# Performance work log

Hardware: AMD Instinct MI355X
Metric: run time of the kernel (lower is better)

Reference implementation:

```python
import jax, jax.numpy as jnp
import numpy as np

B, L, H, E = 16, 4096, 8, 64
IN_CH, OUT_CH, MODES = 512, 512, 64


def setup_inputs() -> dict:
    key = jax.random.key(0)
    kq, kk, kv, k1, k2 = jax.random.split(key, 5)
    scale = 1.0 / (IN_CH * OUT_CH)
    q = jax.random.normal(kq, (B, L, H, E), jnp.float32)
    k = jax.random.normal(kk, (B, L, H, E), jnp.float32)
    v = jax.random.normal(kv, (B, L, H, E), jnp.float32)
    mask = jnp.zeros((B, L), jnp.bool_)
    # learned params: (heads=8, in_ch//8, out_ch//8, modes), torch.rand init * scale
    w1 = scale * jax.random.uniform(k1, (8, IN_CH // 8, OUT_CH // 8, MODES), jnp.float32)
    w2 = scale * jax.random.uniform(k2, (8, IN_CH // 8, OUT_CH // 8, MODES), jnp.float32)
    return {"q": q, "k": k, "v": v, "mask": mask, "w1": w1, "w2": w2}


def reference(q, k, v, mask, w1, w2):
    # q: [B, L, H, E]; k, v, mask unused by the original forward.
    Bq, Lq, Hq, Eq = q.shape
    modes = w1.shape[-1]
    x = jnp.transpose(q, (0, 2, 3, 1))          # [B, H, E, L]
    x_ft = jnp.fft.rfft(x, axis=-1)             # [B, H, E, L//2+1] complex64
    # mode_select_method='else' => index = [0..modes-1], wi == i, so the
    # per-mode gather/einsum/scatter loop collapses to a slice + batched einsum.
    sel = x_ft[..., :modes]                     # [B, H, E_in, modes]
    wc = w1 + 1j * w2                           # [H, E_in, E_out, modes] complex
    out_modes = jnp.einsum('bhim,hiom->bhom', sel, wc)  # [B, H, E_out, modes]
    nfreq = Lq // 2 + 1
    out_ft = jnp.zeros((Bq, Hq, w1.shape[2], nfreq), jnp.complex64)
    out_ft = out_ft.at[..., :modes].set(out_modes)
    x_out = jnp.fft.irfft(out_ft, n=Lq, axis=-1)  # [B, H, E_out, L] float32
    return x_out
```

## Files before the change

kernel.cpp:

```cpp
#include <hip/hip_runtime.h>
#include <math.h>

#define NB 16
#define NL 4096
#define NH 8
#define NI 64
#define NO 64
#define NM 64
#define STEP 1.5339807878856412e-3f

using bf16_t = __bf16;
using bf16x8 = __attribute__((ext_vector_type(8))) __bf16;
using f32x16 = __attribute__((ext_vector_type(16))) float;

#define LDW 136
#define TMC 128

__global__ __launch_bounds__(256) void k_tab(bf16_t* __restrict__ Thi,
                                             bf16_t* __restrict__ Tlo,
                                             bf16_t* __restrict__ Tfhi,
                                             bf16_t* __restrict__ Tflo) {
  const int gid = blockIdx.x * 256 + threadIdx.x;
  {
    const int l = gid >> 7, mc = gid & 127, m = mc >> 1;
    const int p = (m * l) & 4095;
    const float c = cosf((float)p * STEP);
    const float s = cosf((float)((p + 3072) & 4095) * STEP);
    const float val = (mc & 1) ? -s : c;
    const bf16_t hi = (bf16_t)val;
    Thi[gid] = hi;
    Tlo[gid] = (bf16_t)(val - (float)hi);
  }
  {
    const int mc = gid >> 12, l = gid & 4095, m = mc >> 1;
    const int p = (m * l) & 4095;
    const float c = cosf((float)p * STEP);
    const float s = cosf((float)((p + 3072) & 4095) * STEP);
    const float val = (mc & 1) ? -s : c;
    const bf16_t hi = (bf16_t)val;
    Tfhi[gid] = hi;
    Tflo[gid] = (bf16_t)(val - (float)hi);
  }
}

__global__ __launch_bounds__(256) void k_fwd(const float* __restrict__ q,
                                             float* __restrict__ partial,
                                             const bf16_t* __restrict__ Tfhi,
                                             const bf16_t* __restrict__ Tflo,
                                             int LCF, int KCH) {
  const int lc = blockIdx.x, h = blockIdx.y, b = blockIdx.z;
  const int t = threadIdx.x;
  __shared__ uint32_t Bh[64][33], Bl[64][33];

  const int w = t >> 6, lane = t & 63;
  const int arow = lane & 31;
  const int kh = (lane >> 5) << 3;
  const int lp = t & 31;
  const int i0 = (t >> 5) << 3;

  f32x16 acc[2] = {};

  const int lbase0 = lc * KCH;
  const bf16_t* Ah = Tfhi + (size_t)(w * 32 + arow) * NL + lbase0 + kh;
  const bf16_t* Al = Tflo + (size_t)(w * 32 + arow) * NL + lbase0 + kh;

  for (int ks = 0; ks < KCH; ks += 64) {
    __syncthreads();
    {
      const int l0 = lbase0 + ks + (lp << 1);
      const float* qp = q + (((size_t)b * NL + l0) * NH + h) * NI + i0;
      const float4 a0 = *(const float4*)qp;
      const float4 a1 = *(const float4*)(qp + 4);
      const float4 b0 = *(const float4*)(qp + NH * NI);
      const float4 b1 = *(const float4*)(qp + NH * NI + 4);
      const float va[8] = {a0.x, a0.y, a0.z, a0.w, a1.x, a1.y, a1.z, a1.w};
      const float vb[8] = {b0.x, b0.y, b0.z, b0.w, b1.x, b1.y, b1.z, b1.w};
#pragma unroll
      for (int j = 0; j < 8; ++j) {
        const bf16_t h0 = (bf16_t)va[j], h1 = (bf16_t)vb[j];
        const bf16_t g0 = (bf16_t)(va[j] - (float)h0);
        const bf16_t g1 = (bf16_t)(vb[j] - (float)h1);
        union { bf16_t u[2]; uint32_t w32; } ph, pl;
        ph.u[0] = h0; ph.u[1] = h1;
        pl.u[0] = g0; pl.u[1] = g1;
        Bh[i0 + j][lp] = ph.w32;
        Bl[i0 + j][lp] = pl.w32;
      }
    }
    __syncthreads();
#pragma unroll
    for (int kk = 0; kk < 4; ++kk) {
      const bf16x8 ah = *(const bf16x8*)(Ah + ks + kk * 16);
      const bf16x8 al = *(const bf16x8*)(Al + ks + kk * 16);
      const int wd = (kk * 16 + kh) >> 1;
      const bf16x8 bh0 = *(const bf16x8*)&Bh[arow][wd];
      const bf16x8 bl0 = *(const bf16x8*)&Bl[arow][wd];
      const bf16x8 bh1 = *(const bf16x8*)&Bh[arow + 32][wd];
      const bf16x8 bl1 = *(const bf16x8*)&Bl[arow + 32][wd];
#define MM(a, bb, c) c = __builtin_amdgcn_mfma_f32_32x32x16_bf16(a, bb, c, 0, 0, 0)
      MM(ah, bh0, acc[0]); MM(ah, bl0, acc[0]); MM(al, bh0, acc[0]);
      MM(ah, bh1, acc[1]); MM(ah, bl1, acc[1]); MM(al, bh1, acc[1]);
#undef MM
    }
  }

  float* pdst = partial + (((size_t)b * NH + h) * LCF + lc) * (NM * NI * 2);
#pragma unroll
  for (int ihf = 0; ihf < 2; ++ihf)
#pragma unroll
    for (int r = 0; r < 16; ++r) {
      const int mc = w * 32 + (r & 3) + 8 * (r >> 2) + 4 * (lane >> 5);
      const int i = arow + ihf * 32;
      pdst[(mc >> 1) * (NI * 2) + i * 2 + (mc & 1)] = acc[ihf][r];
    }
}

__global__ __launch_bounds__(256) void k_mix(const float* __restrict__ partial,
                                             const float* __restrict__ w1,
                                             const float* __restrict__ w2,
                                             float* __restrict__ out2, int LCF) {
  const int og = blockIdx.x, h = blockIdx.y, b = blockIdx.z;
  const int t = threadIdx.x;
  __shared__ float sel_s[2][64][65];

  const float* src = partial + ((size_t)b * NH + h) * LCF * (NM * NI * 2);
  for (int u = t; u < NM * NI * 2; u += 256) {
    float v = 0.f;
    for (int lcx = 0; lcx < LCF; ++lcx) v += src[(size_t)lcx * (NM * NI * 2) + u];
    sel_s[u & 1][(u >> 1) & 63][u >> 7] = v;
  }
  __syncthreads();

  const int o = og * 16 + (t >> 4);
  const int mt = t & 15;
  float ar[4] = {0.f, 0.f, 0.f, 0.f}, ai[4] = {0.f, 0.f, 0.f, 0.f};
  for (int i = 0; i < NI; ++i) {
    const float* w1p = w1 + (((size_t)h * NI + i) * NO + o) * NM;
    const float* w2p = w2 + (((size_t)h * NI + i) * NO + o) * NM;
#pragma unroll
    for (int k = 0; k < 4; ++k) {
      const int m = mt + (k << 4);
      const float re = sel_s[0][i][m];
      const float im = sel_s[1][i][m];
      const float a = w1p[m];
      const float bb = w2p[m];
      ar[k] = fmaf(re, a, ar[k]);
      ar[k] = fmaf(-im, bb, ar[k]);
      ai[k] = fmaf(re, bb, ai[k]);
      ai[k] = fmaf(im, a, ai[k]);
    }
  }
  float2* dst = (float2*)out2 + ((size_t)b * NH + h) * (NM * NO);
#pragma unroll
  for (int k = 0; k < 4; ++k)
    dst[(mt + (k << 4)) * NO + o] = make_float2(ar[k], ai[k]);
}

__global__ __launch_bounds__(256) void k_inv(const float* __restrict__ out2,
                                             const bf16_t* __restrict__ Thi,
                                             const bf16_t* __restrict__ Tlo,
                                             float* __restrict__ xout) {
  const int lb = blockIdx.x, h = blockIdx.y, b = blockIdx.z;
  const int t = threadIdx.x;
  __shared__ bf16_t Whi[64 * LDW];
  __shared__ bf16_t Wlo[64 * LDW];

  {
    const float2* src = (const float2*)out2 + ((size_t)b * NH + h) * (NM * NO);
    for (int u = t; u < NM * NO; u += 256) {
      const int m = u >> 6, o = u & 63;
      const float fac = (m == 0 ? 1.0f : 2.0f) * (1.0f / 4096.0f);
      const float2 cc = src[u];
      const float re = cc.x * fac, im = cc.y * fac;
      const bf16_t reh = (bf16_t)re, imh = (bf16_t)im;
      Whi[o * LDW + 2 * m] = reh;
      Whi[o * LDW + 2 * m + 1] = imh;
      Wlo[o * LDW + 2 * m] = (bf16_t)(re - (float)reh);
      Wlo[o * LDW + 2 * m + 1] = (bf16_t)(im - (float)imh);
    }
  }
  __syncthreads();

  const int w = t >> 6, lane = t & 63;
  const int lrow = lane & 31;
  const int kh = (lane >> 5) << 3;
  const int lwave = (lb << 8) + (w << 6);

  f32x16 acc[2][2] = {};

#pragma unroll
  for (int ks = 0; ks < 8; ++ks) {
    const int kb = ks * 16 + kh;
    const bf16x8 ah0 = *(const bf16x8*)&Whi[lrow * LDW + kb];
    const bf16x8 ah1 = *(const bf16x8*)&Whi[(lrow + 32) * LDW + kb];
    const bf16x8 al0 = *(const bf16x8*)&Wlo[lrow * LDW + kb];
    const bf16x8 al1 = *(const bf16x8*)&Wlo[(lrow + 32) * LDW + kb];
    const size_t r0 = (size_t)(lwave + lrow) * TMC + kb;
    const size_t r1 = (size_t)(lwave + 32 + lrow) * TMC + kb;
    const bf16x8 bh0 = *(const bf16x8*)&Thi[r0];
    const bf16x8 bh1 = *(const bf16x8*)&Thi[r1];
    const bf16x8 bl0 = *(const bf16x8*)&Tlo[r0];
    const bf16x8 bl1 = *(const bf16x8*)&Tlo[r1];
#define MM(a, bb, c) c = __builtin_amdgcn_mfma_f32_32x32x16_bf16(a, bb, c, 0, 0, 0)
    MM(ah0, bh0, acc[0][0]); MM(ah0, bl0, acc[0][0]); MM(al0, bh0, acc[0][0]);
    MM(ah0, bh1, acc[0][1]); MM(ah0, bl1, acc[0][1]); MM(al0, bh1, acc[0][1]);
    MM(ah1, bh0, acc[1][0]); MM(ah1, bl0, acc[1][0]); MM(al1, bh0, acc[1][0]);
    MM(ah1, bh1, acc[1][1]); MM(ah1, bl1, acc[1][1]); MM(al1, bh1, acc[1][1]);
#undef MM
  }

  float* obase = xout + ((size_t)b * NH + h) * NO * (size_t)NL;
#pragma unroll
  for (int of = 0; of < 2; ++of)
#pragma unroll
    for (int lf = 0; lf < 2; ++lf) {
      const int lg = lwave + lf * 32 + lrow;
#pragma unroll
      for (int r = 0; r < 16; ++r) {
        const int o = of * 32 + (r & 3) + 8 * (r >> 2) + 4 * (lane >> 5);
        obase[(size_t)o * NL + lg] = acc[of][lf][r];
      }
    }
}

extern "C" void kernel_launch(void* const* d_in, const int* in_sizes, int n_in,
                              void* d_out, int out_size, void* d_ws, size_t ws_size,
                              hipStream_t stream) {
  const float* q  = (const float*)d_in[0];
  const float* w1 = (const float*)d_in[4];
  const float* w2 = (const float*)d_in[5];
  float* out = (float*)d_out;

  const size_t out2Elems = (size_t)NB * NH * NM * NO * 2;
  const size_t tE = 524288;
  const size_t tabFloats = (4 * tE) / 2;
  int LCF = 1;
  const int cands[4] = {8, 4, 2, 1};
  for (int ci = 0; ci < 4; ++ci) {
    const size_t pe = (size_t)NB * NH * cands[ci] * NM * NI * 2;
    if ((pe + out2Elems + tabFloats) * sizeof(float) <= ws_size) { LCF = cands[ci]; break; }
  }
  const size_t partialElems = (size_t)NB * NH * LCF * NM * NI * 2;
  float* partial = (float*)d_ws;
  float* out2 = partial + partialElems;
  bf16_t* Thi = (bf16_t*)(out2 + out2Elems);
  bf16_t* Tlo = Thi + tE;
  bf16_t* Tfhi = Tlo + tE;
  bf16_t* Tflo = Tfhi + tE;

  dim3 blk(256);
  k_tab<<<dim3((unsigned)(tE / 256)), blk, 0, stream>>>(Thi, Tlo, Tfhi, Tflo);
  k_fwd<<<dim3(LCF, NH, NB), blk, 0, stream>>>(q, partial, Tfhi, Tflo, LCF, NL / LCF);
  k_mix<<<dim3(4, NH, NB), blk, 0, stream>>>(partial, w1, w2, out2, LCF);
  k_inv<<<dim3(16, NH, NB), blk, 0, stream>>>(out2, Thi, Tlo, out);
}
```

Before: 486.9 us.

## Move spectral mode mixing onto bf16 split-precision MFMA with pre-laid weights

Replaces the scalar FMA mode-mixing kernel with a reduce/pack kernel plus an MFMA kernel that batches over B per (mode, head). Weights are split into hi/lo bf16 with complex-interleaved K and laid out per mode, and the partial sums are reduced and packed into matching hi/lo A operands. It also changes how k_fwd stages q into shared memory, so each thread reads one channel across 16 positions. This adds two extra kernel launches and workspace, and keeps accuracy only through the 3-term bf16 split.

```diff
diff --git a/kernel.cpp b/kernel.cpp
--- a/kernel.cpp
+++ b/kernel.cpp
@@ -11,10 +11,16 @@
 
 using bf16_t = __bf16;
 using bf16x8 = __attribute__((ext_vector_type(8))) __bf16;
+using f32x4  = __attribute__((ext_vector_type(4))) float;
 using f32x16 = __attribute__((ext_vector_type(16))) float;
 
 #define LDW 136
 #define TMC 128
+
+__device__ __forceinline__ uint32_t pk2(float x, float y) {
+  union { bf16_t b[2]; uint32_t u; } r;
+  r.b[0] = (bf16_t)x; r.b[1] = (bf16_t)y; return r.u;
+}
 
 __global__ __launch_bounds__(256) void k_tab(bf16_t* __restrict__ Thi,
                                              bf16_t* __restrict__ Tlo,
@@ -43,6 +49,37 @@
   }
 }
 
+__global__ __launch_bounds__(256) void k_wt(const float* __restrict__ w1,
+                                            const float* __restrict__ w2,
+                                            bf16_t* __restrict__ Bwhi,
+                                            bf16_t* __restrict__ Bwlo) {
+  const int it = blockIdx.x;
+  const int h = blockIdx.y;
+  const int og = blockIdx.z;
+  const int t = threadIdx.x;
+  const int m = t & 63, os = t >> 6;
+  const int o = og * 4 + os;
+
+  union { bf16_t a[32]; bf16x8 v[4]; } hib, lob;
+#pragma unroll
+  for (int ii = 0; ii < 16; ++ii) {
+    const int i = it * 16 + ii;
+    const size_t widx = (((size_t)h * NI + i) * NO + o) * NM + m;
+    const float a = w1[widx];
+    const float bv = -w2[widx];
+    const bf16_t ah = (bf16_t)a;
+    const bf16_t bh = (bf16_t)bv;
+    hib.a[2 * ii] = ah;     lob.a[2 * ii] = (bf16_t)(a - (float)ah);
+    hib.a[2 * ii + 1] = bh; lob.a[2 * ii + 1] = (bf16_t)(bv - (float)bh);
+  }
+  const size_t dst = (((size_t)h * NM + m) * NO + o) * 128 + it * 32;
+#pragma unroll
+  for (int j = 0; j < 4; ++j) {
+    *(bf16x8*)(Bwhi + dst + j * 8) = hib.v[j];
+    *(bf16x8*)(Bwlo + dst + j * 8) = lob.v[j];
+  }
+}
+
 __global__ __launch_bounds__(256) void k_fwd(const float* __restrict__ q,
                                              float* __restrict__ partial,
                                              const bf16_t* __restrict__ Tfhi,
@@ -50,41 +87,38 @@
                                              int LCF, int KCH) {
   const int lc = blockIdx.x, h = blockIdx.y, b = blockIdx.z;
   const int t = threadIdx.x;
-  __shared__ uint32_t Bh[64][33], Bl[64][33];
+  __shared__ uint32_t Bh[64][34], Bl[64][34];
 
   const int w = t >> 6, lane = t & 63;
   const int arow = lane & 31;
   const int kh = (lane >> 5) << 3;
-  const int lp = t & 31;
-  const int i0 = (t >> 5) << 3;
+  const int iA = t & 63;
+  const int wv = t >> 6;
 
   f32x16 acc[2] = {};
 
   const int lbase0 = lc * KCH;
   const bf16_t* Ah = Tfhi + (size_t)(w * 32 + arow) * NL + lbase0 + kh;
   const bf16_t* Al = Tflo + (size_t)(w * 32 + arow) * NL + lbase0 + kh;
+  bf16_t* BhP = (bf16_t*)Bh;
+  bf16_t* BlP = (bf16_t*)Bl;
 
   for (int ks = 0; ks < KCH; ks += 64) {
     __syncthreads();
     {
-      const int l0 = lbase0 + ks + (lp << 1);
-      const float* qp = q + (((size_t)b * NL + l0) * NH + h) * NI + i0;
-      const float4 a0 = *(const float4*)qp;
-      const float4 a1 = *(const float4*)(qp + 4);
-      const float4 b0 = *(const float4*)(qp + NH * NI);
-      const float4 b1 = *(const float4*)(qp + NH * NI + 4);
-      const float va[8] = {a0.x, a0.y, a0.z, a0.w, a1.x, a1.y, a1.z, a1.w};
-      const float vb[8] = {b0.x, b0.y, b0.z, b0.w, b1.x, b1.y, b1.z, b1.w};
-#pragma unroll
-      for (int j = 0; j < 8; ++j) {
-        const bf16_t h0 = (bf16_t)va[j], h1 = (bf16_t)vb[j];
-        const bf16_t g0 = (bf16_t)(va[j] - (float)h0);
-        const bf16_t g1 = (bf16_t)(vb[j] - (float)h1);
-        union { bf16_t u[2]; uint32_t w32; } ph, pl;
-        ph.u[0] = h0; ph.u[1] = h1;
-        pl.u[0] = g0; pl.u[1] = g1;
-        Bh[i0 + j][lp] = ph.w32;
-        Bl[i0 + j][lp] = pl.w32;
+      const float* qp =
+          q + (((size_t)b * NL + (lbase0 + ks + wv * 16)) * NH + h) * NI + iA;
+      float vv[16];
+#pragma unroll
+      for (int c = 0; c < 16; ++c) vv[c] = qp[(size_t)c * NH * NI];
+#pragma unroll
+      for (int c = 0; c < 16; ++c) {
+        const int lloc = wv * 16 + c;
+        const bf16_t hi = (bf16_t)vv[c];
+        const bf16_t lo = (bf16_t)(vv[c] - (float)hi);
+        const int w16 = (iA * 34 + (lloc >> 1)) * 2 + (lloc & 1);
+        BhP[w16] = hi;
+        BlP[w16] = lo;
       }
     }
     __syncthreads();
@@ -115,45 +149,69 @@
     }
 }
 
-__global__ __launch_bounds__(256) void k_mix(const float* __restrict__ partial,
-                                             const float* __restrict__ w1,
-                                             const float* __restrict__ w2,
-                                             float* __restrict__ out2, int LCF) {
-  const int og = blockIdx.x, h = blockIdx.y, b = blockIdx.z;
+__global__ __launch_bounds__(256) void k_red(const float* __restrict__ partial,
+                                             uint32_t* __restrict__ Ahi,
+                                             uint32_t* __restrict__ Alo,
+                                             uint32_t* __restrict__ Aimhi,
+                                             uint32_t* __restrict__ Aimlo,
+                                             int LCF) {
+  const int gid = blockIdx.x * 256 + threadIdx.x;
+  const int i = gid & 63, b = (gid >> 6) & 15, m = (gid >> 10) & 63, h = gid >> 16;
+  const float* src = partial + ((size_t)b * NH + h) * (size_t)LCF * (NM * NI * 2) +
+                     m * (NI * 2) + i * 2;
+  float re = 0.f, im = 0.f;
+  for (int lc = 0; lc < LCF; ++lc) {
+    const float2 v = *(const float2*)(src + (size_t)lc * (NM * NI * 2));
+    re += v.x; im += v.y;
+  }
+  const bf16_t reh = (bf16_t)re, imh = (bf16_t)im;
+  const float rel = re - (float)reh, iml = im - (float)imh;
+  Ahi[gid] = pk2(re, im);
+  Alo[gid] = pk2(rel, iml);
+  Aimhi[gid] = pk2(im, -re);
+  Aimlo[gid] = pk2(iml, -rel);
+}
+
+__global__ __launch_bounds__(256) void k_mix(const uint32_t* __restrict__ Ahi,
+                                             const uint32_t* __restrict__ Alo,
+                                             const uint32_t* __restrict__ Aimhi,
+                                             const uint32_t* __restrict__ Aimlo,
+                                             const bf16_t* __restrict__ Bwhi,
+                                             const bf16_t* __restrict__ Bwlo,
+                                             float* __restrict__ out2) {
+  const int m = blockIdx.x, h = blockIdx.y;
   const int t = threadIdx.x;
-  __shared__ float sel_s[2][64][65];
-
-  const float* src = partial + ((size_t)b * NH + h) * LCF * (NM * NI * 2);
-  for (int u = t; u < NM * NI * 2; u += 256) {
-    float v = 0.f;
-    for (int lcx = 0; lcx < LCF; ++lcx) v += src[(size_t)lcx * (NM * NI * 2) + u];
-    sel_s[u & 1][(u >> 1) & 63][u >> 7] = v;
-  }
-  __syncthreads();
-
-  const int o = og * 16 + (t >> 4);
-  const int mt = t & 15;
-  float ar[4] = {0.f, 0.f, 0.f, 0.f}, ai[4] = {0.f, 0.f, 0.f, 0.f};
-  for (int i = 0; i < NI; ++i) {
-    const float* w1p = w1 + (((size_t)h * NI + i) * NO + o) * NM;
-    const float* w2p = w2 + (((size_t)h * NI + i) * NO + o) * NM;
-#pragma unroll
-    for (int k = 0; k < 4; ++k) {
-      const int m = mt + (k << 4);
-      const float re = sel_s[0][i][m];
-      const float im = sel_s[1][i][m];
-      const float a = w1p[m];
-      const float bb = w2p[m];
-      ar[k] = fmaf(re, a, ar[k]);
-      ar[k] = fmaf(-im, bb, ar[k]);
-      ai[k] = fmaf(re, bb, ai[k]);
-      ai[k] = fmaf(im, a, ai[k]);
-    }
-  }
-  float2* dst = (float2*)out2 + ((size_t)b * NH + h) * (NM * NO);
-#pragma unroll
-  for (int k = 0; k < 4; ++k)
-    dst[(mt + (k << 4)) * NO + o] = make_float2(ar[k], ai[k]);
+  const int of = t >> 6, lane = t & 63;
+  const int row = lane & 15;
+  const int kg = (lane >> 4) << 3;
+
+  const size_t abase = (((size_t)h * NM + m) * 16 + row) * 64;
+  const size_t bbase = (((size_t)h * NM + m) * NO + of * 16 + row) * 128;
+
+  f32x4 accre = {}, accim = {};
+#pragma unroll
+  for (int ks = 0; ks < 4; ++ks) {
+    const int k0 = ks * 32 + kg;
+    const bf16x8 ah  = *(const bf16x8*)((const bf16_t*)Ahi + abase * 2 + k0);
+    const bf16x8 al  = *(const bf16x8*)((const bf16_t*)Alo + abase * 2 + k0);
+    const bf16x8 aih = *(const bf16x8*)((const bf16_t*)Aimhi + abase * 2 + k0);
+    const bf16x8 ail = *(const bf16x8*)((const bf16_t*)Aimlo + abase * 2 + k0);
+    const bf16x8 bh  = *(const bf16x8*)(Bwhi + bbase + k0);
+    const bf16x8 bl  = *(const bf16x8*)(Bwlo + bbase + k0);
+#define MM16(a, bb, c) c = __builtin_amdgcn_mfma_f32_16x16x32_bf16(a, bb, c, 0, 0, 0)
+    MM16(ah, bh, accre); MM16(al, bh, accre); MM16(ah, bl, accre);
+    MM16(aih, bh, accim); MM16(ail, bh, accim); MM16(aih, bl, accim);
+#undef MM16
+  }
+
+  float2* o2 = (float2*)out2;
+  const int o = of * 16 + (lane & 15);
+#pragma unroll
+  for (int r = 0; r < 4; ++r) {
+    const int b = ((lane >> 4) << 2) + r;
+    o2[((size_t)b * NH + h) * (NM * NO) + m * NO + o] =
+        make_float2(accre[r], accim[r]);
+  }
 }
 
 __global__ __launch_bounds__(256) void k_inv(const float* __restrict__ out2,
@@ -233,12 +291,15 @@
 
   const size_t out2Elems = (size_t)NB * NH * NM * NO * 2;
   const size_t tE = 524288;
-  const size_t tabFloats = (4 * tE) / 2;
+  const size_t aW = 524288;
+  const size_t bE = 4194304;
+  const size_t fixedFloats = out2Elems + (4 * tE) / 2 + 4 * aW + (2 * bE) / 2;
+
   int LCF = 1;
   const int cands[4] = {8, 4, 2, 1};
   for (int ci = 0; ci < 4; ++ci) {
     const size_t pe = (size_t)NB * NH * cands[ci] * NM * NI * 2;
-    if ((pe + out2Elems + tabFloats) * sizeof(float) <= ws_size) { LCF = cands[ci]; break; }
+    if ((pe + fixedFloats) * sizeof(float) <= ws_size) { LCF = cands[ci]; break; }
   }
   const size_t partialElems = (size_t)NB * NH * LCF * NM * NI * 2;
   float* partial = (float*)d_ws;
@@ -247,10 +308,18 @@
   bf16_t* Tlo = Thi + tE;
   bf16_t* Tfhi = Tlo + tE;
   bf16_t* Tflo = Tfhi + tE;
+  uint32_t* Ahi = (uint32_t*)(Tflo + tE);
+  uint32_t* Alo = Ahi + aW;
+  uint32_t* Aimhi = Alo + aW;
+  uint32_t* Aimlo = Aimhi + aW;
+  bf16_t* Bwhi = (bf16_t*)(Aimlo + aW);
+  bf16_t* Bwlo = Bwhi + bE;
 
   dim3 blk(256);
   k_tab<<<dim3((unsigned)(tE / 256)), blk, 0, stream>>>(Thi, Tlo, Tfhi, Tflo);
+  k_wt<<<dim3(4, NH, 16), blk, 0, stream>>>(w1, w2, Bwhi, Bwlo);
   k_fwd<<<dim3(LCF, NH, NB), blk, 0, stream>>>(q, partial, Tfhi, Tflo, LCF, NL / LCF);
-  k_mix<<<dim3(4, NH, NB), blk, 0, stream>>>(partial, w1, w2, out2, LCF);
+  k_red<<<dim3(2048), blk, 0, stream>>>(partial, Ahi, Alo, Aimhi, Aimlo, LCF);
+  k_mix<<<dim3(NM, NH), blk, 0, stream>>>(Ahi, Alo, Aimhi, Aimlo, Bwhi, Bwlo, out2);
   k_inv<<<dim3(16, NH, NB), blk, 0, stream>>>(out2, Thi, Tlo, out);
 }
```

Measured after the change: 432.5 us. 1.13x faster.
